# Performance work log

Hardware: AMD Instinct MI355X
Metric: run time of the kernel (lower is better)

## Reference

```python
import jax, jax.numpy as jnp
import numpy as np

N, E, P, L, F, H, T = 6000, 72000, 2, 2, 64, 4, 64
NF_MLP = 256
DH = F // H
M = (L + 1) ** 2  # 9 spherical components for max_degree=2
DEG = np.array([l for l in range(L + 1) for _ in range(2 * l + 1)])  # degree of each m-component
EPS = 1e-6


def _deg_dense(x, W):
    # x: (n,P,M,Fin); W: (P,L+1,Fin,Fout). Separate feature mixing per (parity, degree),
    return jnp.einsum('npmf,pmfg->npmg', x, W[:, DEG])


def _eqv_layernorm(x):
    # Equivariant LayerNorm (no scale/bias): center the scalar (l=0) channel over features,
    # then divide each (parity, degree) block by the RMS (over features) of its per-degree norm.
    s = x[:, :, 0:1, :]
    x = x.at[:, :, 0:1, :].set(s - s.mean(axis=-1, keepdims=True))
    n2 = jnp.stack([(x[:, :, l * l:(l + 1) * (l + 1), :] ** 2).sum(axis=2) / (2 * l + 1)
                    for l in range(L + 1)], axis=2)  # (n,P,L+1,F)
    rms = jnp.sqrt(n2.mean(axis=-1, keepdims=True) + EPS)  # (n,P,L+1,1)
    return x / rms[:, :, DEG, :]


def _modulate(x, scale, shift):
    # modulate_E3adaLN: x * (1 + gamma) with gamma broadcast per degree; shift only on l=0 (scalar).
    y = x * (1.0 + scale[:, :, DEG, :])
    return y.at[:, :, 0:1, :].add(shift)


def _gate(factor, t):
    # broadcast_equivariant_multiplication: per-(parity,degree,feature) factor broadcast over m.
    return factor[:, :, DEG, :] * t


def _eqv_gelu(x):
    s = x[:, 0:1, 0:1, :]
    mask = jnp.abs(s) > 1e-4
    safe = jnp.where(mask, s, 1.0)
    g = jnp.where(mask, jax.nn.gelu(safe) / safe, 0.5)
    return x * g


def _forward(features_nodes, features_edges, features_time, cutoff_value,
             ln_t_scale, ln_t_bias, W_c, b_c, Wq, Wk, Wv, Wo, We_qk, We_v, W1, W2,
             src_idx, dst_idx):
    n = features_nodes.shape[0]
    # ---- AdaLN conditioning from time features ----
    mu = features_time.mean(-1, keepdims=True)
    var = ((features_time - mu) ** 2).mean(-1, keepdims=True)
    c = (features_time - mu) / jnp.sqrt(var + EPS) * ln_t_scale + ln_t_bias
    c = jax.nn.silu(c) @ W_c + b_c  # (n, 4*F*(L+1)*P + 2F)
    a = F * (L + 1) * P  # 384
    g1, b1, a1, g2, b2, a2 = jnp.split(c, [a, a + F, 2 * a + F, 3 * a + F, 3 * a + 2 * F], axis=-1)
    g1 = g1.reshape(n, P, L + 1, F); b1 = b1.reshape(n, 1, 1, F); a1 = a1.reshape(n, P, L + 1, F)
    g2 = g2.reshape(n, P, L + 1, F); b2 = b2.reshape(n, 1, 1, F); a2 = a2.reshape(n, P, L + 1, F)
    x_pre = _modulate(_eqv_layernorm(features_nodes), g1, b1)
    # ---- sparse graph equivariant self-attention ----
    q = _deg_dense(x_pre, Wq).reshape(n, P, M, H, DH)
    k = _deg_dense(x_pre, Wk).reshape(n, P, M, H, DH)
    v = _deg_dense(x_pre, Wv).reshape(n, P, M, H, DH)
    e_qk = jnp.einsum('eomf,fg->eomg', features_edges, We_qk).reshape(-1, 1, M, H, DH)
    e_v = jnp.einsum('eomf,fg->eomg', features_edges, We_v).reshape(-1, 1, M, H, DH)
    qe = q[dst_idx]
    ke = k[src_idx] * e_qk  # relative positional encoding on keys
    ve = v[src_idx] * e_v   # relative positional encoding on values
    logits = jnp.einsum('epmhd,epmhd->eh', qe, ke) / np.sqrt(P * M * DH)  # rotation-invariant
    lmax = jax.ops.segment_max(logits, dst_idx, num_segments=n)
    w = jnp.exp(logits - lmax[dst_idx]) * cutoff_value[:, None]  # cutoff-masked softmax weight
    denom = jax.ops.segment_sum(w, dst_idx, num_segments=n)
    attn = w / (denom[dst_idx] + 1e-9)  # (E,H)
    out = jax.ops.segment_sum(attn[:, None, None, :, None] * ve, dst_idx, num_segments=n)
    out = _deg_dense(out.reshape(n, P, M, F), Wo)
    # fallback to pre-attention features where segment_mean(cutoff) ~ 0 (isolated nodes)
    cnt = jax.ops.segment_sum(jnp.ones_like(cutoff_value), dst_idx, num_segments=n)
    mean_cut = jax.ops.segment_sum(cutoff_value, dst_idx, num_segments=n) / jnp.maximum(cnt, 1.0)
    post = jnp.where(mean_cut.reshape(-1, 1, 1, 1) < 1e-5, x_pre, out)
    x = features_nodes + _gate(a1, post)
    # ---- equivariant MLP ----
    x_pre2 = _modulate(_eqv_layernorm(x), g2, b2)
    h = _eqv_gelu(_deg_dense(x_pre2, W1))
    x = x + _gate(a2, _deg_dense(h, W2))
    return x  # node features; edge features pass through unchanged


def setup_inputs():
    key = jax.random.key(0)
    ks = jax.random.split(key, 16)
    CDIM = 4 * F * (L + 1) * P + 2 * F  # 1664
    return {
        'features_nodes': jax.random.normal(ks[0], (N, P, M, F), jnp.float32),
        'features_edges': jax.random.normal(ks[1], (E, 1, M, F), jnp.float32),
        'features_time': jax.random.normal(ks[2], (N, T), jnp.float32),
        'cutoff_value': jax.random.uniform(ks[3], (E,), jnp.float32),
        'ln_t_scale': jnp.ones((T,), jnp.float32),
        'ln_t_bias': jnp.zeros((T,), jnp.float32),
        'W_c': jax.random.normal(ks[4], (T, CDIM), jnp.float32) * 0.02,
        'b_c': jnp.zeros((CDIM,), jnp.float32),
        'Wq': jax.random.normal(ks[5], (P, L + 1, F, F), jnp.float32) / np.sqrt(F),
        'Wk': jax.random.normal(ks[6], (P, L + 1, F, F), jnp.float32) / np.sqrt(F),
        'Wv': jax.random.normal(ks[7], (P, L + 1, F, F), jnp.float32) / np.sqrt(F),
        'Wo': jax.random.normal(ks[8], (P, L + 1, F, F), jnp.float32) / np.sqrt(F),
        'We_qk': jax.random.normal(ks[9], (F, F), jnp.float32) / np.sqrt(F),
        'We_v': jax.random.normal(ks[10], (F, F), jnp.float32) / np.sqrt(F),
        'W1': jax.random.normal(ks[11], (P, L + 1, F, NF_MLP), jnp.float32) / np.sqrt(F),
        'W2': jax.random.normal(ks[12], (P, L + 1, NF_MLP, F), jnp.float32) / np.sqrt(NF_MLP),
        'src_idx': jax.random.randint(ks[13], (E,), 0, N),
        'dst_idx': jax.random.randint(ks[14], (E,), 0, N),
    }


def reference(features_nodes, features_edges, features_time, cutoff_value,
              ln_t_scale, ln_t_bias, W_c, b_c, Wq, Wk, Wv, Wo, We_qk, We_v, W1, W2,
              src_idx, dst_idx):
    return _forward(features_nodes, features_edges, features_time, cutoff_value,
                    ln_t_scale, ln_t_bias, W_c, b_c, Wq, Wk, Wv, Wo, We_qk, We_v, W1, W2,
                    src_idx, dst_idx)
```

## Files before the change

kernel.cpp:

```cpp
#include <hip/hip_runtime.h>
#include <hip/hip_fp16.h>
#include <math.h>


#define NN 6000
#define EE 72000

__device__ __forceinline__ float wsum(float v) {
#pragma unroll
  for (int o = 32; o >= 1; o >>= 1) v += __shfl_xor(v, o, 64);
  return v;
}
__device__ __forceinline__ int deg_of(int m) { return (m == 0) ? 0 : ((m < 4) ? 1 : 2); }
__device__ __forceinline__ unsigned fenc(float x) {
  unsigned u = __float_as_uint(x);
  return (u & 0x80000000u) ? ~u : (u | 0x80000000u);
}
__device__ __forceinline__ float fdec(unsigned k) {
  unsigned u = (k & 0x80000000u) ? (k & 0x7fffffffu) : ~k;
  return __uint_as_float(u);
}

__global__ __launch_bounds__(256) void k_ln_t(const float* __restrict__ ft,
                                              const float* __restrict__ lns,
                                              const float* __restrict__ lnb,
                                              float* __restrict__ sbuf) {
  int w = (blockIdx.x * 256 + threadIdx.x) >> 6;
  int lane = threadIdx.x & 63;
  float t = ft[(size_t)w * 64 + lane];
  float mu = wsum(t) * (1.f / 64.f);
  float d = t - mu;
  float var = wsum(d * d) * (1.f / 64.f);
  float cin = d * rsqrtf(var + 1e-6f) * lns[lane] + lnb[lane];
  sbuf[(size_t)w * 64 + lane] = cin / (1.f + expf(-cin));
}

__global__ __launch_bounds__(256) void k_cond_mm(const float* __restrict__ sbuf,
                                                 const float* __restrict__ Wc,
                                                 const float* __restrict__ bc,
                                                 float* __restrict__ c) {
  __shared__ __align__(16) float st[8 * 64];
  int n0 = blockIdx.x * 8;
  for (int i = threadIdx.x; i < 512; i += 256) st[i] = sbuf[(size_t)n0 * 64 + i];
  __syncthreads();
  for (int jj = threadIdx.x; jj < 1664; jj += 256) {
    float acc[8] = {0, 0, 0, 0, 0, 0, 0, 0};
#pragma unroll 8
    for (int k2 = 0; k2 < 64; k2++) {
      float wv = Wc[(size_t)k2 * 1664 + jj];
#pragma unroll
      for (int nd = 0; nd < 8; nd++) acc[nd] += st[nd * 64 + k2] * wv;
    }
    float b = bc[jj];
#pragma unroll
    for (int nd = 0; nd < 8; nd++) c[(size_t)(n0 + nd) * 1664 + jj] = acc[nd] + b;
  }
}

__global__ __launch_bounds__(256) void k_lnmod(const float* __restrict__ xin,
                                               const float* __restrict__ c,
                                               float* __restrict__ xout,
                                               int goff, int boff) {
  int w = (blockIdx.x * 256 + threadIdx.x) >> 6;
  int lane = threadIdx.x & 63;
  int n = w >> 1, p = w & 1;
  const float* xb = xin + (size_t)w * 576 + lane;
  float x0 = xb[0], x1 = xb[64], x2 = xb[128], x3 = xb[192], x4 = xb[256];
  float x5 = xb[320], x6 = xb[384], x7 = xb[448], x8 = xb[512];
  float mu = wsum(x0) * (1.f / 64.f);
  x0 -= mu;
  float n20 = x0 * x0;
  float n21 = (x1 * x1 + x2 * x2 + x3 * x3) * (1.f / 3.f);
  float n22 = (x4 * x4 + x5 * x5 + x6 * x6 + x7 * x7 + x8 * x8) * (1.f / 5.f);
  n20 = wsum(n20) * (1.f / 64.f);
  n21 = wsum(n21) * (1.f / 64.f);
  n22 = wsum(n22) * (1.f / 64.f);
  float i0 = rsqrtf(n20 + 1e-6f), i1 = rsqrtf(n21 + 1e-6f), i2 = rsqrtf(n22 + 1e-6f);
  const float* cb = c + (size_t)n * 1664;
  float g0 = 1.f + cb[goff + p * 192 + lane];
  float g1 = 1.f + cb[goff + p * 192 + 64 + lane];
  float g2 = 1.f + cb[goff + p * 192 + 128 + lane];
  float bsh = cb[boff + lane];
  float* ob = xout + (size_t)w * 576 + lane;
  ob[0] = x0 * i0 * g0 + bsh;
  ob[64] = x1 * i1 * g1;
  ob[128] = x2 * i1 * g1;
  ob[192] = x3 * i1 * g1;
  ob[256] = x4 * i2 * g2;
  ob[320] = x5 * i2 * g2;
  ob[384] = x6 * i2 * g2;
  ob[448] = x7 * i2 * g2;
  ob[512] = x8 * i2 * g2;
}

__global__ __launch_bounds__(256) void k_count(const int* __restrict__ dst_idx,
                                               const float* __restrict__ cutoff,
                                               float* __restrict__ cnt,
                                               float* __restrict__ cutsum) {
  int e = blockIdx.x * 256 + threadIdx.x;
  if (e >= EE) return;
  int d = dst_idx[e];
  unsafeAtomicAdd(cnt + d, 1.f);
  unsafeAtomicAdd(cutsum + d, cutoff[e]);
}

__global__ __launch_bounds__(1024) void k_scan(const float* __restrict__ cnt,
                                               int* __restrict__ rowptr,
                                               int* __restrict__ fillc) {
  __shared__ int part[1024];
  int t = threadIdx.x;
  int base = t * 6;
  int lc[6];
  int s = 0;
#pragma unroll
  for (int i = 0; i < 6; i++) {
    int idx = base + i;
    int vv = (idx < NN) ? (int)(cnt[idx] + 0.5f) : 0;
    lc[i] = s;
    s += vv;
  }
  part[t] = s;
  __syncthreads();
  for (int o = 1; o < 1024; o <<= 1) {
    int vv = (t >= o) ? part[t - o] : 0;
    __syncthreads();
    part[t] += vv;
    __syncthreads();
  }
  int ex = (t == 0) ? 0 : part[t - 1];
#pragma unroll
  for (int i = 0; i < 6; i++) {
    int idx = base + i;
    if (idx < NN) {
      int p = ex + lc[i];
      rowptr[idx] = p;
      fillc[idx] = p;
    }
  }
  if (t == 1023) rowptr[NN] = part[1023];
}

__global__ __launch_bounds__(256) void k_fill(const int* __restrict__ dst_idx,
                                              const int* __restrict__ src_idx,
                                              const float* __restrict__ cutoff,
                                              int* __restrict__ fillc,
                                              int* __restrict__ eids,
                                              int* __restrict__ dsts,
                                              int* __restrict__ srcs,
                                              float* __restrict__ cuts) {
  int e = blockIdx.x * 256 + threadIdx.x;
  if (e >= EE) return;
  int d = dst_idx[e];
  int pos = atomicAdd(fillc + d, 1);
  eids[pos] = e;
  dsts[pos] = d;
  srcs[pos] = src_idx[e];
  cuts[pos] = cutoff[e];
}

__global__ __launch_bounds__(192) void k_qkv2(const float* __restrict__ xpre,
                                              const float* __restrict__ Wq,
                                              const float* __restrict__ Wk,
                                              const float* __restrict__ Wv,
                                              __half* __restrict__ qh,
                                              __half* __restrict__ kh,
                                              __half* __restrict__ vh) {
  __shared__ __align__(16) float xt[16 * 64];
  int pm = blockIdx.y;
  int p = pm / 9, dm = deg_of(pm % 9);
  int n0 = blockIdx.x * 16;
  int mat = threadIdx.x >> 6;
  int g = threadIdx.x & 63;
  for (int i = threadIdx.x; i < 1024; i += 192) {
    int r = i >> 6, f = i & 63;
    xt[i] = xpre[((size_t)(n0 + r) * 18 + pm) * 64 + f];
  }
  const float* Wsel = (mat == 0) ? Wq : ((mat == 1) ? Wk : Wv);
  const float* Wb = Wsel + (size_t)(p * 3 + dm) * 4096;
  __half* ob = (mat == 0) ? qh : ((mat == 1) ? kh : vh);
  float wreg[64];
#pragma unroll
  for (int f = 0; f < 64; f++) wreg[f] = Wb[f * 64 + g];
  __syncthreads();
  for (int r = 0; r < 16; r++) {
    float acc = 0.f;
#pragma unroll
    for (int f4 = 0; f4 < 16; f4++) {
      float4 a = *(const float4*)(xt + r * 64 + f4 * 4);
      acc += a.x * wreg[4 * f4] + a.y * wreg[4 * f4 + 1] + a.z * wreg[4 * f4 + 2] +
             a.w * wreg[4 * f4 + 3];
    }
    ob[((size_t)(n0 + r) * 18 + pm) * 64 + g] = __float2half(acc);
  }
}

__global__ __launch_bounds__(256) void k_edge(const float* __restrict__ fe,
                                              const float* __restrict__ Weqk,
                                              const float* __restrict__ Wev,
                                              const __half* __restrict__ qh,
                                              const __half* __restrict__ kh,
                                              const int* __restrict__ eids,
                                              const int* __restrict__ dsts,
                                              const int* __restrict__ srcs,
                                              __half* __restrict__ evh,
                                              float* __restrict__ logw,
                                              unsigned* __restrict__ lmax) {
  __shared__ __align__(16) float ft[16 * 576];
  int s0 = blockIdx.x * 16;
  int g = threadIdx.x & 63;
  int w = threadIdx.x >> 6;
  float wq[64], wv[64];
#pragma unroll
  for (int f = 0; f < 64; f++) {
    wq[f] = Weqk[f * 64 + g];
    wv[f] = Wev[f * 64 + g];
  }
  {
    int sl = threadIdx.x >> 4, j = threadIdx.x & 15;
    const float* sp = fe + (size_t)eids[s0 + sl] * 576;
#pragma unroll
    for (int i = 0; i < 9; i++) {
      *(float4*)(ft + sl * 576 + i * 64 + j * 4) = *(const float4*)(sp + i * 64 + j * 4);
    }
  }
  __syncthreads();
  for (int ss = 0; ss < 4; ss++) {
    int sl = w * 4 + ss;
    int s = s0 + sl;
    float eq[9];
#pragma unroll
    for (int m = 0; m < 9; m++) {
      float eqm = 0.f, evm = 0.f;
#pragma unroll
      for (int f4 = 0; f4 < 16; f4++) {
        float4 a = *(const float4*)(ft + sl * 576 + m * 64 + f4 * 4);
        eqm += a.x * wq[4 * f4] + a.y * wq[4 * f4 + 1] + a.z * wq[4 * f4 + 2] +
               a.w * wq[4 * f4 + 3];
        evm += a.x * wv[4 * f4] + a.y * wv[4 * f4 + 1] + a.z * wv[4 * f4 + 2] +
               a.w * wv[4 * f4 + 3];
      }
      eq[m] = eqm;
      evh[(size_t)s * 576 + m * 64 + g] = __float2half(evm);
    }
    int dst = __builtin_amdgcn_readfirstlane(dsts[s]);
    int src = __builtin_amdgcn_readfirstlane(srcs[s]);
    const __half* qb = qh + (size_t)dst * 1152 + g;
    const __half* kb = kh + (size_t)src * 1152 + g;
    float lacc = 0.f;
#pragma unroll
    for (int m = 0; m < 9; m++) {
      float qk = __half2float(qb[m * 64]) * __half2float(kb[m * 64]) +
                 __half2float(qb[m * 64 + 576]) * __half2float(kb[m * 64 + 576]);
      lacc += eq[m] * qk;
    }
    lacc *= 0.05892556509887896f;
    lacc += __shfl_xor(lacc, 8, 64);
    lacc += __shfl_xor(lacc, 4, 64);
    lacc += __shfl_xor(lacc, 2, 64);
    lacc += __shfl_xor(lacc, 1, 64);
    if ((g & 15) == 0) {
      int h = g >> 4;
      logw[(size_t)s * 4 + h] = lacc;
      atomicMax(lmax + (size_t)dst * 4 + h, fenc(lacc));
    }
  }
}

__global__ __launch_bounds__(256) void k_expw2(float* __restrict__ logw,
                                               const unsigned* __restrict__ lmax,
                                               const int* __restrict__ dsts,
                                               const float* __restrict__ cuts,
                                               float* __restrict__ denom) {
  int t = blockIdx.x * 256 + threadIdx.x;
  int s = t >> 2, h = t & 3;
  int dst = dsts[s];
  float wv = expf(logw[t] - fdec(lmax[(size_t)dst * 4 + h])) * cuts[s];
  logw[t] = wv;
  unsafeAtomicAdd(denom + (size_t)dst * 4 + h, wv);
}

__global__ __launch_bounds__(256) void k_fagg2(const __half* __restrict__ evh,
                                               const __half* __restrict__ vh,
                                               const int* __restrict__ srcs,
                                               const int* __restrict__ rowptr,
                                               const float* __restrict__ logw,
                                               const float* __restrict__ denom,
                                               float* __restrict__ attn_out) {
  int dst = (blockIdx.x * 256 + threadIdx.x) >> 6;
  int g = threadIdx.x & 63;
  int e0 = __builtin_amdgcn_readfirstlane(rowptr[dst]);
  int e1 = __builtin_amdgcn_readfirstlane(rowptr[dst + 1]);
  float invd = 1.f / (denom[(size_t)dst * 4 + (g >> 4)] + 1e-9f);
  float acc[18];
#pragma unroll
  for (int i = 0; i < 18; i++) acc[i] = 0.f;
  for (int s = e0; s < e1; s++) {
    float attn = logw[(size_t)s * 4 + (g >> 4)] * invd;
    int src = __builtin_amdgcn_readfirstlane(srcs[s]);
    const __half* eb = evh + (size_t)s * 576 + g;
    const __half* vb = vh + (size_t)src * 1152 + g;
#pragma unroll
    for (int m = 0; m < 9; m++) {
      float sc = attn * __half2float(eb[m * 64]);
      acc[m] += sc * __half2float(vb[m * 64]);
      acc[m + 9] += sc * __half2float(vb[m * 64 + 576]);
    }
  }
  float* ob = attn_out + (size_t)dst * 1152 + g;
#pragma unroll
  for (int m = 0; m < 9; m++) {
    ob[m * 64] = acc[m];
    ob[m * 64 + 576] = acc[m + 9];
  }
}

__global__ __launch_bounds__(256) void k_wo_post3(const float* __restrict__ attn_out,
                                                  const float* __restrict__ Wo,
                                                  const float* __restrict__ xpre,
                                                  const float* __restrict__ fnodes,
                                                  const float* __restrict__ c,
                                                  const float* __restrict__ cnt,
                                                  const float* __restrict__ cutsum,
                                                  float* __restrict__ out) {
  __shared__ __align__(16) float xt[16 * 64];
  int pm = blockIdx.y;
  int p = pm / 9, dm = deg_of(pm % 9);
  int n0 = blockIdx.x * 16;
  int g = threadIdx.x & 63, w = threadIdx.x >> 6;
  for (int i = threadIdx.x; i < 1024; i += 256) {
    int r = i >> 6, f = i & 63;
    xt[i] = attn_out[((size_t)(n0 + r) * 18 + pm) * 64 + f];
  }
  const float* Wb = Wo + (size_t)(p * 3 + dm) * 4096;
  float wreg[64];
#pragma unroll
  for (int f = 0; f < 64; f++) wreg[f] = Wb[f * 64 + g];
  __syncthreads();
  for (int i = 0; i < 4; i++) {
    int r = w * 4 + i;
    int n = n0 + r;
    float acc = 0.f;
#pragma unroll
    for (int f4 = 0; f4 < 16; f4++) {
      float4 a = *(const float4*)(xt + r * 64 + f4 * 4);
      acc += a.x * wreg[4 * f4] + a.y * wreg[4 * f4 + 1] + a.z * wreg[4 * f4 + 2] +
             a.w * wreg[4 * f4 + 3];
    }
    float mc = cutsum[n] / fmaxf(cnt[n], 1.f);
    size_t idx = ((size_t)n * 18 + pm) * 64 + g;
    float post = (mc < 1e-5f) ? xpre[idx] : acc;
    float a1v = c[(size_t)n * 1664 + 448 + (p * 3 + dm) * 64 + g];
    out[idx] = fnodes[idx] + a1v * post;
  }
}

__global__ __launch_bounds__(256) void k_mlp1v2(const float* __restrict__ xp2,
                                                const float* __restrict__ W1,
                                                float* __restrict__ h) {
  __shared__ __align__(16) float xt[16 * 64];
  int pm = blockIdx.y;
  int p = pm / 9, dm = deg_of(pm % 9);
  int n0 = blockIdx.x * 16;
  int w = threadIdx.x >> 6, g = threadIdx.x & 63;
  const float* w1b = W1 + (size_t)(p * 3 + dm) * 16384;
  float w1reg[64];
#pragma unroll
  for (int f = 0; f < 64; f++) w1reg[f] = w1b[(size_t)f * 256 + w * 64 + g];
  for (int i = threadIdx.x; i < 1024; i += 256) {
    int r = i >> 6, f = i & 63;
    xt[i] = xp2[((size_t)(n0 + r) * 18 + pm) * 64 + f];
  }
  __syncthreads();
  for (int r = 0; r < 16; r++) {
    float a0 = 0.f, a1 = 0.f, a2 = 0.f, a3 = 0.f;
#pragma unroll
    for (int f4 = 0; f4 < 16; f4 += 4) {
      float4 x0 = *(const float4*)(xt + r * 64 + f4 * 4);
      float4 x1 = *(const float4*)(xt + r * 64 + f4 * 4 + 4);
      float4 x2 = *(const float4*)(xt + r * 64 + f4 * 4 + 8);
      float4 x3 = *(const float4*)(xt + r * 64 + f4 * 4 + 12);
      a0 += x0.x * w1reg[4 * f4] + x0.y * w1reg[4 * f4 + 1] + x0.z * w1reg[4 * f4 + 2] +
            x0.w * w1reg[4 * f4 + 3];
      a1 += x1.x * w1reg[4 * f4 + 4] + x1.y * w1reg[4 * f4 + 5] +
            x1.z * w1reg[4 * f4 + 6] + x1.w * w1reg[4 * f4 + 7];
      a2 += x2.x * w1reg[4 * f4 + 8] + x2.y * w1reg[4 * f4 + 9] +
            x2.z * w1reg[4 * f4 + 10] + x2.w * w1reg[4 * f4 + 11];
      a3 += x3.x * w1reg[4 * f4 + 12] + x3.y * w1reg[4 * f4 + 13] +
            x3.z * w1reg[4 * f4 + 14] + x3.w * w1reg[4 * f4 + 15];
    }
    h[((size_t)(n0 + r) * 18 + pm) * 256 + w * 64 + g] = (a0 + a1) + (a2 + a3);
  }
}

__global__ __launch_bounds__(256) void k_gate2(const float* __restrict__ h,
                                               float* __restrict__ gatebuf) {
  int n = blockIdx.x;
  int j = threadIdx.x;
  float s = h[(size_t)n * 4608 + j];
  float gt = (fabsf(s) > 1e-4f)
                 ? 0.5f * (1.f + tanhf(0.7978845608028654f * (s + 0.044715f * s * s * s)))
                 : 0.5f;
  gatebuf[(size_t)n * 256 + j] = gt;
}

__global__ __launch_bounds__(256) void k_mlp2v2(const float* __restrict__ h,
                                                const float* __restrict__ W2,
                                                const float* __restrict__ gatebuf,
                                                const float* __restrict__ c,
                                                float* __restrict__ out) {
  __shared__ __align__(16) float ht[16 * 256];
  __shared__ float po[4][16 * 64];
  int pm = blockIdx.y;
  int p = pm / 9, dm = deg_of(pm % 9);
  int n0 = blockIdx.x * 16;
  int w = threadIdx.x >> 6, g = threadIdx.x & 63;
  const float* w2b = W2 + (size_t)(p * 3 + dm) * 16384;
  float w2reg[64];
#pragma unroll
  for (int k = 0; k < 64; k++) w2reg[k] = w2b[(size_t)(w * 64 + k) * 64 + g];
  for (int i = threadIdx.x; i < 4096; i += 256) {
    int r = i >> 8, k = i & 255;
    ht[i] = h[((size_t)(n0 + r) * 18 + pm) * 256 + k] *
            gatebuf[(size_t)(n0 + r) * 256 + k];
  }
  __syncthreads();
  for (int r = 0; r < 16; r++) {
    float a0 = 0.f, a1 = 0.f, a2 = 0.f, a3 = 0.f;
#pragma unroll
    for (int k4 = 0; k4 < 16; k4 += 4) {
      float4 h0 = *(const float4*)(ht + r * 256 + w * 64 + k4 * 4);
      float4 h1 = *(const float4*)(ht + r * 256 + w * 64 + k4 * 4 + 4);
      float4 h2 = *(const float4*)(ht + r * 256 + w * 64 + k4 * 4 + 8);
      float4 h3 = *(const float4*)(ht + r * 256 + w * 64 + k4 * 4 + 12);
      a0 += h0.x * w2reg[4 * k4] + h0.y * w2reg[4 * k4 + 1] + h0.z * w2reg[4 * k4 + 2] +
            h0.w * w2reg[4 * k4 + 3];
      a1 += h1.x * w2reg[4 * k4 + 4] + h1.y * w2reg[4 * k4 + 5] +
            h1.z * w2reg[4 * k4 + 6] + h1.w * w2reg[4 * k4 + 7];
      a2 += h2.x * w2reg[4 * k4 + 8] + h2.y * w2reg[4 * k4 + 9] +
            h2.z * w2reg[4 * k4 + 10] + h2.w * w2reg[4 * k4 + 11];
      a3 += h3.x * w2reg[4 * k4 + 12] + h3.y * w2reg[4 * k4 + 13] +
            h3.z * w2reg[4 * k4 + 14] + h3.w * w2reg[4 * k4 + 15];
    }
    po[w][r * 64 + g] = (a0 + a1) + (a2 + a3);
  }
  __syncthreads();
  for (int i = threadIdx.x; i < 1024; i += 256) {
    int r = i >> 6, gg = i & 63;
    float s2 = po[0][i] + po[1][i] + po[2][i] + po[3][i];
    int n = n0 + r;
    size_t idx = ((size_t)n * 18 + pm) * 64 + gg;
    out[idx] += c[(size_t)n * 1664 + 1280 + (p * 3 + dm) * 64 + gg] * s2;
  }
}

#define OFF_C 0UL
#define OFF_XPRE 39936000UL
#define OFF_QH 67584000UL
#define OFF_KH 81408000UL
#define OFF_VH 95232000UL
#define OFF_EVH 109056000UL
#define OFF_ATTN 67584000UL
#define OFF_H 67584000UL
#define OFF_SBUF 192000000UL
#define OFF_LOGW 193536000UL
#define OFF_LMAX 194688000UL
#define OFF_DENOM 194784000UL
#define OFF_CNT 194880000UL
#define OFF_CUTSUM 194904000UL
#define OFF_ROWPTR 194928000UL
#define OFF_FILLC 194952064UL
#define OFF_EIDS 194976064UL
#define OFF_DSTS 195264064UL
#define OFF_SRCS 195552064UL
#define OFF_CUTS 195840064UL
#define OFF_GATE 196128064UL
#define WS_NEEDED 202272064UL

extern "C" void kernel_launch(void* const* d_in, const int* in_sizes, int n_in,
                              void* d_out, int out_size, void* d_ws, size_t ws_size,
                              hipStream_t stream) {
  const float* f_nodes = (const float*)d_in[0];
  const float* f_edges = (const float*)d_in[1];
  const float* f_time = (const float*)d_in[2];
  const float* cutoff = (const float*)d_in[3];
  const float* ln_s = (const float*)d_in[4];
  const float* ln_b = (const float*)d_in[5];
  const float* W_c = (const float*)d_in[6];
  const float* b_c = (const float*)d_in[7];
  const float* Wq = (const float*)d_in[8];
  const float* Wk = (const float*)d_in[9];
  const float* Wv = (const float*)d_in[10];
  const float* Wo = (const float*)d_in[11];
  const float* We_qk = (const float*)d_in[12];
  const float* We_v = (const float*)d_in[13];
  const float* W1 = (const float*)d_in[14];
  const float* W2 = (const float*)d_in[15];
  const int* src_idx = (const int*)d_in[16];
  const int* dst_idx = (const int*)d_in[17];
  float* out = (float*)d_out;
  char* ws = (char*)d_ws;
  if (ws_size < WS_NEEDED) return;

  float* c = (float*)(ws + OFF_C);
  float* xpre = (float*)(ws + OFF_XPRE);
  __half* qh = (__half*)(ws + OFF_QH);
  __half* kh = (__half*)(ws + OFF_KH);
  __half* vh = (__half*)(ws + OFF_VH);
  __half* evh = (__half*)(ws + OFF_EVH);
  float* attn_out = (float*)(ws + OFF_ATTN);
  float* hbuf = (float*)(ws + OFF_H);
  float* sbuf = (float*)(ws + OFF_SBUF);
  float* logw = (float*)(ws + OFF_LOGW);
  unsigned* lmax = (unsigned*)(ws + OFF_LMAX);
  float* denom = (float*)(ws + OFF_DENOM);
  float* cnt = (float*)(ws + OFF_CNT);
  float* cutsum = (float*)(ws + OFF_CUTSUM);
  int* rowptr = (int*)(ws + OFF_ROWPTR);
  int* fillc = (int*)(ws + OFF_FILLC);
  int* eids = (int*)(ws + OFF_EIDS);
  int* dsts = (int*)(ws + OFF_DSTS);
  int* srcs = (int*)(ws + OFF_SRCS);
  float* cuts = (float*)(ws + OFF_CUTS);
  float* gatebuf = (float*)(ws + OFF_GATE);

  hipMemsetAsync(ws + OFF_LMAX, 0, 240000, stream);

  k_ln_t<<<1500, 256, 0, stream>>>(f_time, ln_s, ln_b, sbuf);
  k_count<<<282, 256, 0, stream>>>(dst_idx, cutoff, cnt, cutsum);
  k_cond_mm<<<750, 256, 0, stream>>>(sbuf, W_c, b_c, c);
  k_scan<<<1, 1024, 0, stream>>>(cnt, rowptr, fillc);
  k_fill<<<282, 256, 0, stream>>>(dst_idx, src_idx, cutoff, fillc, eids, dsts, srcs,
                                  cuts);
  k_lnmod<<<3000, 256, 0, stream>>>(f_nodes, c, xpre, 0, 384);

  k_qkv2<<<dim3(375, 18), 192, 0, stream>>>(xpre, Wq, Wk, Wv, qh, kh, vh);

  k_edge<<<4500, 256, 0, stream>>>(f_edges, We_qk, We_v, qh, kh, eids, dsts, srcs, evh,
                                   logw, lmax);
  k_expw2<<<1125, 256, 0, stream>>>(logw, lmax, dsts, cuts, denom);
  k_fagg2<<<1500, 256, 0, stream>>>(evh, vh, srcs, rowptr, logw, denom, attn_out);
  k_wo_post3<<<dim3(375, 18), 256, 0, stream>>>(attn_out, Wo, xpre, f_nodes, c, cnt,
                                                cutsum, out);

  k_lnmod<<<3000, 256, 0, stream>>>(out, c, xpre, 832, 1216);
  k_mlp1v2<<<dim3(375, 18), 256, 0, stream>>>(xpre, W1, hbuf);
  k_gate2<<<6000, 256, 0, stream>>>(hbuf, gatebuf);
  k_mlp2v2<<<dim3(375, 18), 256, 0, stream>>>(hbuf, W2, gatebuf, c, out);
}
```

Before: 976.3 us.

## Compute edge feature projections with fp16 MFMA instead of scalar FMA

Replaces the scalar per-thread dot products in the edge kernel with 16x16x32 fp16 MFMA instructions. Each wave handles its own edges, loading edge features straight from global memory, converting them to fp16, and staging the results through per-wave LDS before the attention logit and value store. This is meant to cut the heavy FMA cost of the two 64x64 projections per edge. In exchange it lowers input precision to fp16, wastes 7 of 16 MFMA rows because there are only 9 components, and adds LDS round trips.

```diff
diff --git a/kernel.cpp b/kernel.cpp
--- a/kernel.cpp
+++ b/kernel.cpp
@@ -5,6 +5,9 @@
 
 #define NN 6000
 #define EE 72000
+
+typedef _Float16 f16x8 __attribute__((ext_vector_type(8)));
+typedef float f32x4 __attribute__((ext_vector_type(4)));
 
 __device__ __forceinline__ float wsum(float v) {
 #pragma unroll
@@ -194,54 +197,76 @@
   }
 }
 
-__global__ __launch_bounds__(256) void k_edge(const float* __restrict__ fe,
-                                              const float* __restrict__ Weqk,
-                                              const float* __restrict__ Wev,
-                                              const __half* __restrict__ qh,
-                                              const __half* __restrict__ kh,
-                                              const int* __restrict__ eids,
-                                              const int* __restrict__ dsts,
-                                              const int* __restrict__ srcs,
-                                              __half* __restrict__ evh,
-                                              float* __restrict__ logw,
-                                              unsigned* __restrict__ lmax) {
-  __shared__ __align__(16) float ft[16 * 576];
-  int s0 = blockIdx.x * 16;
-  int g = threadIdx.x & 63;
-  int w = threadIdx.x >> 6;
-  float wq[64], wv[64];
-#pragma unroll
-  for (int f = 0; f < 64; f++) {
-    wq[f] = Weqk[f * 64 + g];
-    wv[f] = Wev[f * 64 + g];
-  }
-  {
-    int sl = threadIdx.x >> 4, j = threadIdx.x & 15;
-    const float* sp = fe + (size_t)eids[s0 + sl] * 576;
-#pragma unroll
-    for (int i = 0; i < 9; i++) {
-      *(float4*)(ft + sl * 576 + i * 64 + j * 4) = *(const float4*)(sp + i * 64 + j * 4);
-    }
-  }
-  __syncthreads();
+__global__ __launch_bounds__(256) void k_edge_mfma(const float* __restrict__ fe,
+                                                   const float* __restrict__ Weqk,
+                                                   const float* __restrict__ Wev,
+                                                   const __half* __restrict__ qh,
+                                                   const __half* __restrict__ kh,
+                                                   const int* __restrict__ eids,
+                                                   const int* __restrict__ dsts,
+                                                   const int* __restrict__ srcs,
+                                                   __half* __restrict__ evh,
+                                                   float* __restrict__ logw,
+                                                   unsigned* __restrict__ lmax) {
+  __shared__ float ldsbuf[4 * 2176];
+  int lane = threadIdx.x & 63;
+  int wid = threadIdx.x >> 6;
+  int r16 = lane & 15;
+  int kg = lane >> 4;
+  f16x8 bfrag[2][4][2];
+#pragma unroll
+  for (int ct = 0; ct < 4; ct++) {
+#pragma unroll
+    for (int ks = 0; ks < 2; ks++) {
+      f16x8 bq, bv;
+#pragma unroll
+      for (int j = 0; j < 8; j++) {
+        int k = ks * 32 + kg * 8 + j;
+        bq[j] = (_Float16)Weqk[(size_t)k * 64 + ct * 16 + r16];
+        bv[j] = (_Float16)Wev[(size_t)k * 64 + ct * 16 + r16];
+      }
+      bfrag[0][ct][ks] = bq;
+      bfrag[1][ct][ks] = bv;
+    }
+  }
+  float* lq = ldsbuf + wid * 2176;
+  float* lv = ldsbuf + wid * 2176 + 1088;
+  int mclamp = (r16 < 9) ? r16 : 8;
+  int s0 = (blockIdx.x * 4 + wid) * 4;
   for (int ss = 0; ss < 4; ss++) {
-    int sl = w * 4 + ss;
-    int s = s0 + sl;
-    float eq[9];
-#pragma unroll
-    for (int m = 0; m < 9; m++) {
-      float eqm = 0.f, evm = 0.f;
-#pragma unroll
-      for (int f4 = 0; f4 < 16; f4++) {
-        float4 a = *(const float4*)(ft + sl * 576 + m * 64 + f4 * 4);
-        eqm += a.x * wq[4 * f4] + a.y * wq[4 * f4 + 1] + a.z * wq[4 * f4 + 2] +
-               a.w * wq[4 * f4 + 3];
-        evm += a.x * wv[4 * f4] + a.y * wv[4 * f4 + 1] + a.z * wv[4 * f4 + 2] +
-               a.w * wv[4 * f4 + 3];
+    int s = s0 + ss;
+    int e = __builtin_amdgcn_readfirstlane(eids[s]);
+    const float* feb = fe + (size_t)e * 576 + mclamp * 64 + kg * 8;
+    f16x8 a0, a1;
+    {
+      float4 p0 = *(const float4*)(feb);
+      float4 p1 = *(const float4*)(feb + 4);
+      float4 p2 = *(const float4*)(feb + 32);
+      float4 p3 = *(const float4*)(feb + 36);
+      a0[0] = (_Float16)p0.x; a0[1] = (_Float16)p0.y;
+      a0[2] = (_Float16)p0.z; a0[3] = (_Float16)p0.w;
+      a0[4] = (_Float16)p1.x; a0[5] = (_Float16)p1.y;
+      a0[6] = (_Float16)p1.z; a0[7] = (_Float16)p1.w;
+      a1[0] = (_Float16)p2.x; a1[1] = (_Float16)p2.y;
+      a1[2] = (_Float16)p2.z; a1[3] = (_Float16)p2.w;
+      a1[4] = (_Float16)p3.x; a1[5] = (_Float16)p3.y;
+      a1[6] = (_Float16)p3.z; a1[7] = (_Float16)p3.w;
+    }
+#pragma unroll
+    for (int ct = 0; ct < 4; ct++) {
+      f32x4 zq = {0.f, 0.f, 0.f, 0.f};
+      zq = __builtin_amdgcn_mfma_f32_16x16x32_f16(a0, bfrag[0][ct][0], zq, 0, 0, 0);
+      zq = __builtin_amdgcn_mfma_f32_16x16x32_f16(a1, bfrag[0][ct][1], zq, 0, 0, 0);
+      f32x4 zv = {0.f, 0.f, 0.f, 0.f};
+      zv = __builtin_amdgcn_mfma_f32_16x16x32_f16(a0, bfrag[1][ct][0], zv, 0, 0, 0);
+      zv = __builtin_amdgcn_mfma_f32_16x16x32_f16(a1, bfrag[1][ct][1], zv, 0, 0, 0);
+#pragma unroll
+      for (int reg = 0; reg < 4; reg++) {
+        lq[(kg * 4 + reg) * 68 + ct * 16 + r16] = zq[reg];
+        lv[(kg * 4 + reg) * 68 + ct * 16 + r16] = zv[reg];
       }
-      eq[m] = eqm;
-      evh[(size_t)s * 576 + m * 64 + g] = __float2half(evm);
-    }
+    }
+    int g = lane;
     int dst = __builtin_amdgcn_readfirstlane(dsts[s]);
     int src = __builtin_amdgcn_readfirstlane(srcs[s]);
     const __half* qb = qh + (size_t)dst * 1152 + g;
@@ -249,9 +274,11 @@
     float lacc = 0.f;
 #pragma unroll
     for (int m = 0; m < 9; m++) {
+      float eqv = lq[m * 68 + g];
+      evh[(size_t)s * 576 + m * 64 + g] = __float2half(lv[m * 68 + g]);
       float qk = __half2float(qb[m * 64]) * __half2float(kb[m * 64]) +
                  __half2float(qb[m * 64 + 576]) * __half2float(kb[m * 64 + 576]);
-      lacc += eq[m] * qk;
+      lacc += eqv * qk;
     }
     lacc *= 0.05892556509887896f;
     lacc += __shfl_xor(lacc, 8, 64);
@@ -535,8 +562,8 @@
 
   k_qkv2<<<dim3(375, 18), 192, 0, stream>>>(xpre, Wq, Wk, Wv, qh, kh, vh);
 
-  k_edge<<<4500, 256, 0, stream>>>(f_edges, We_qk, We_v, qh, kh, eids, dsts, srcs, evh,
-                                   logw, lmax);
+  k_edge_mfma<<<4500, 256, 0, stream>>>(f_edges, We_qk, We_v, qh, kh, eids, dsts, srcs,
+                                        evh, logw, lmax);
   k_expw2<<<1125, 256, 0, stream>>>(logw, lmax, dsts, cuts, denom);
   k_fagg2<<<1500, 256, 0, stream>>>(evh, vh, srcs, rowptr, logw, denom, attn_out);
   k_wo_post3<<<dim3(375, 18), 256, 0, stream>>>(attn_out, Wo, xpre, f_nodes, c, cnt,
```

Result: faster. 920.6 us (-5.7%).
